# Optimization experiments

Hardware: AMD Instinct MI355X
Metric: run time of the kernel (lower is better)

## Reference

```python
import jax, jax.numpy as jnp
import numpy as np

B, T, D = 2, 4096, 768
H = 12
HD = D // H  # 64
SCALE = 1.0 / np.sqrt(HD)


def setup_inputs() -> dict:
    key = jax.random.key(0)
    k1, k2, k3 = jax.random.split(key, 3)
    x = jax.random.normal(k1, (B, T, D), dtype=jnp.float32)
    W_qkv = jax.random.normal(k2, (D, 3 * D), dtype=jnp.float32) * (1.0 / np.sqrt(D))
    b_qkv = jnp.zeros((3 * D,), dtype=jnp.float32)
    W_out = jax.random.normal(k3, (D, D), dtype=jnp.float32) * (1.0 / np.sqrt(D))
    b_out = jnp.zeros((D,), dtype=jnp.float32)
    return {"x": x, "W_qkv": W_qkv, "b_qkv": b_qkv, "W_out": W_out, "b_out": b_out}


def reference(x, W_qkv, b_qkv, W_out, b_out):
    Bx, Tx, C = x.shape
    qkv = x @ W_qkv + b_qkv                                  # [B,T,3D]
    qkv = qkv.reshape(Bx, Tx, 3, H, HD).transpose(2, 0, 3, 1, 4)  # [3,B,H,T,hd]
    q, k, v = qkv[0], qkv[1], qkv[2]
    scores = jnp.einsum('bhqd,bhkd->bhqk', q, k) * SCALE      # [B,H,T,T]
    causal = jnp.tril(jnp.ones((Tx, Tx), dtype=bool))
    scores = jnp.where(causal[None, None], scores, -jnp.inf)
    attn = jax.nn.softmax(scores, axis=-1)
    out = jnp.einsum('bhqk,bhkd->bhqd', attn, v)              # [B,H,T,hd]
    out = out.transpose(0, 2, 1, 3).reshape(Bx, Tx, C)        # [B,T,D]
    return out @ W_out + b_out
```

## Files before the change

kernel.cpp:

```cpp
#include <hip/hip_runtime.h>
#include <cstdint>
#include <cstddef>

typedef _Float16 f16x8 __attribute__((ext_vector_type(8)));
typedef _Float16 f16x4 __attribute__((ext_vector_type(4)));
typedef float    f32x4 __attribute__((ext_vector_type(4)));

#define AS_GLOBAL __attribute__((address_space(1)))
#define AS_LDS    __attribute__((address_space(3)))

__device__ __forceinline__ void load16_to_lds(const _Float16* g, _Float16* l) {
    __builtin_amdgcn_global_load_lds((const AS_GLOBAL void*)g, (AS_LDS void*)l, 16, 0, 0);
}

#define BB   2
#define TT   4096
#define DD   768
#define NH   12
#define HDIM 64
#define D3   2304
#define SC2  (0.125f * 1.44269504088896f)

__global__ __launch_bounds__(256) void prep(const float* __restrict__ x,
                                            _Float16* __restrict__ Xh,
                                            const float* __restrict__ Wqkv,
                                            _Float16* __restrict__ Wqkvt,
                                            const float* __restrict__ Wout,
                                            _Float16* __restrict__ Wot) {
    const int bid = blockIdx.x, tid = threadIdx.x;
    if (bid < 6144) {
        const int i = bid * 1024 + tid * 4;
        float4 v = *(const float4*)(x + i);
        f16x4 h;
        h[0] = (_Float16)v.x; h[1] = (_Float16)v.y;
        h[2] = (_Float16)v.z; h[3] = (_Float16)v.w;
        *(f16x4*)(Xh + i) = h;
        return;
    }
    __shared__ float tile[32][33];
    const float* in; _Float16* out; int C, bx, by;
    if (bid < 7872) {
        const int t = bid - 6144;
        in = Wqkv; out = Wqkvt; C = 2304;
        bx = (t % 72) * 32; by = (t / 72) * 32;
    } else {
        const int t = bid - 7872;
        in = Wout; out = Wot; C = 768;
        bx = (t % 24) * 32; by = (t / 24) * 32;
    }
    const int R = 768;
    const int tx = tid & 31, ty = tid >> 5;
#pragma unroll
    for (int j = 0; j < 32; j += 8)
        tile[ty + j][tx] = in[(size_t)(by + ty + j) * C + bx + tx];
    __syncthreads();
#pragma unroll
    for (int j = 0; j < 32; j += 8)
        out[(size_t)(bx + ty + j) * R + by + tx] = (_Float16)tile[tx][ty + j];
}

template <typename OutT>
__device__ __forceinline__ void gemm_body(const _Float16* __restrict__ A,
                                          const _Float16* __restrict__ Bt,
                                          const float* __restrict__ bias, bool bias_row,
                                          OutT* __restrict__ C, int N, int K,
                                          int m0, int n0,
                                          _Float16* As, _Float16* Bs) {
    const int tid  = threadIdx.x;
    const int wave = tid >> 6, lane = tid & 63, quad = lane >> 4, l16 = lane & 15;
    const int wm = (wave & 1) * 64, wn = (wave >> 1) * 64;
    const int rowc = lane >> 2, part = lane & 3;

    f32x4 acc[4][4];
#pragma unroll
    for (int i = 0; i < 4; ++i)
#pragma unroll
        for (int n = 0; n < 4; ++n) acc[i][n] = f32x4{0.f, 0.f, 0.f, 0.f};

    for (int k0 = 0; k0 < K; k0 += 32) {
        __syncthreads();
#pragma unroll
        for (int cc = 0; cc < 2; ++cc) {
            const int ch = wave * 2 + cc;
            load16_to_lds(A  + (size_t)(m0 + ch * 16 + rowc) * K + k0 + part * 8,
                          As + ch * 512);
            load16_to_lds(Bt + (size_t)(n0 + ch * 16 + rowc) * K + k0 + part * 8,
                          Bs + ch * 512);
        }
        __syncthreads();
#pragma unroll
        for (int i = 0; i < 4; ++i) {
            f16x8 a = *(const f16x8*)(As + (wm + i * 16 + l16) * 32 + quad * 8);
#pragma unroll
            for (int n = 0; n < 4; ++n) {
                f16x8 b = *(const f16x8*)(Bs + (wn + n * 16 + l16) * 32 + quad * 8);
                acc[i][n] = __builtin_amdgcn_mfma_f32_16x16x32_f16(a, b, acc[i][n], 0, 0, 0);
            }
        }
    }
#pragma unroll
    for (int i = 0; i < 4; ++i)
#pragma unroll
        for (int n = 0; n < 4; ++n)
#pragma unroll
            for (int r = 0; r < 4; ++r) {
                const int row = m0 + wm + i * 16 + quad * 4 + r;
                const int col = n0 + wn + n * 16 + l16;
                const float bv = bias_row ? bias[row] : bias[col];
                C[(size_t)row * N + col] = (OutT)(acc[i][n][r] + bv);
            }
}

__global__ __launch_bounds__(256) void gemm_qkv(const _Float16* __restrict__ Xh,
                                                const _Float16* __restrict__ Wqkvt,
                                                const float* __restrict__ bqkv,
                                                _Float16* __restrict__ QKh,
                                                _Float16* __restrict__ VtG) {
    __shared__ __align__(16) _Float16 As[128 * 32];
    __shared__ __align__(16) _Float16 Bs[128 * 32];
    const int bid = blockIdx.x;
    if (bid < 768) {
        const int bx = bid % 12, by = bid / 12;
        gemm_body<_Float16>(Xh, Wqkvt, bqkv, false, QKh, 1536, DD,
                            by * 128, bx * 128, As, Bs);
    } else {
        const int t = bid - 768;
        const int bx = t % 64, by = t / 64;
        gemm_body<_Float16>(Wqkvt + (size_t)1536 * DD, Xh, bqkv + 1536, true, VtG,
                            8192, DD, by * 128, bx * 128, As, Bs);
    }
}

__global__ __launch_bounds__(256) void gemm_out(const _Float16* __restrict__ A,
                                                const _Float16* __restrict__ Bt,
                                                const float* __restrict__ bias,
                                                float* __restrict__ C) {
    __shared__ __align__(16) _Float16 As[128 * 32];
    __shared__ __align__(16) _Float16 Bs[128 * 32];
    gemm_body<float>(A, Bt, bias, false, C, DD, DD,
                     (int)blockIdx.y * 128, (int)blockIdx.x * 128, As, Bs);
}

__global__ __launch_bounds__(128) void attn_kernel(const _Float16* __restrict__ qk,
                                                   const _Float16* __restrict__ vt,
                                                   _Float16* __restrict__ ao) {
    __shared__ __align__(16) _Float16 Ks[2][64 * 64];
    __shared__ __align__(16) _Float16 Vs[2][64 * 64];
    __shared__ __align__(16) _Float16 Ps[2][32 * 64];
    const int b = blockIdx.z, h = blockIdx.y;
    const int tid = threadIdx.x;
    const int wave = tid >> 6, lane = tid & 63, quad = lane >> 4, l16 = lane & 15;

    f16x8 ones;
#pragma unroll
    for (int j = 0; j < 8; ++j) ones[j] = (_Float16)1.0f;

    const _Float16* pK[4];
    const _Float16* pV[4];
#pragma unroll
    for (int p = 0; p < 4; ++p) {
        const int j  = wave * 32 + p * 8 + (lane >> 3);
        const int sig = (j & 15) * 4 + (j >> 4);
        const int cdk = (lane & 7) ^ (j & 7);
        pK[p] = qk + (size_t)(b * TT + sig) * 1536 + DD + h * HDIM + cdk * 8;
        pV[p] = vt + (size_t)(h * HDIM + j) * 8192 + b * TT + cdk * 8;
    }
    auto stage = [&](int buf, int k0) {
#pragma unroll
        for (int p = 0; p < 4; ++p) {
            load16_to_lds(pK[p] + (size_t)k0 * 1536, Ks[buf] + (wave * 32 + p * 8) * 64);
            load16_to_lds(pV[p] + k0,                Vs[buf] + (wave * 32 + p * 8) * 64);
        }
    };

    _Float16* pw[2][4];
#pragma unroll
    for (int mi = 0; mi < 2; ++mi)
#pragma unroll
        for (int r = 0; r < 4; ++r) {
            const int row = mi * 16 + quad * 4 + r;
            pw[mi][r] = Ps[wave] + row * 64 + (((l16 >> 1) ^ (row & 7)) * 8) + (l16 & 1) * 4;
        }
    const _Float16* pr[2][2];
#pragma unroll
    for (int mi = 0; mi < 2; ++mi)
#pragma unroll
        for (int kh = 0; kh < 2; ++kh) {
            const int row = mi * 16 + l16;
            pr[mi][kh] = Ps[wave] + row * 64 + (((kh * 4 + quad) ^ (row & 7)) * 8);
        }

    auto process = [&](int qt) {
        const int q0 = qt * 64;
        const int nkt = qt + 1;
        f16x8 aq[2][2];
#pragma unroll
        for (int mi = 0; mi < 2; ++mi) {
            const int q = q0 + wave * 32 + mi * 16 + l16;
            const _Float16* qp = qk + (size_t)(b * TT + q) * 1536 + h * HDIM + quad * 8;
            const _Float16 sc = (_Float16)SC2;
            aq[mi][0] = *(const f16x8*)qp * sc;
            aq[mi][1] = *(const f16x8*)(qp + 32) * sc;
        }
        f32x4 o[2][4], lac[2];
#pragma unroll
        for (int mi = 0; mi < 2; ++mi) {
#pragma unroll
            for (int n = 0; n < 4; ++n) o[mi][n] = f32x4{0.f, 0.f, 0.f, 0.f};
            lac[mi] = f32x4{0.f, 0.f, 0.f, 0.f};
        }

        __syncthreads();
        stage(0, 0);
        int cur = 0;
        for (int kt = 0; kt < nkt; ++kt) {
            __syncthreads();
            if (kt + 1 < nkt) stage(cur ^ 1, (kt + 1) * 64);

            f32x4 s[2][4];
#pragma unroll
            for (int mi = 0; mi < 2; ++mi)
#pragma unroll
                for (int n = 0; n < 4; ++n) s[mi][n] = f32x4{0.f, 0.f, 0.f, 0.f};
#pragma unroll
            for (int kh = 0; kh < 2; ++kh)
#pragma unroll
                for (int n = 0; n < 4; ++n) {
                    const int pos = (kh * 4 + quad) ^ (l16 & 7);
                    f16x8 bk = *(const f16x8*)(Ks[cur] + (n * 16 + l16) * 64 + pos * 8);
#pragma unroll
                    for (int mi = 0; mi < 2; ++mi)
                        s[mi][n] = __builtin_amdgcn_mfma_f32_16x16x32_f16(aq[mi][kh], bk,
                                                                          s[mi][n], 0, 0, 0);
                }

            if (kt == nkt - 1) {
#pragma unroll
                for (int n = 0; n < 4; ++n) {
                    const int kg = kt * 64 + l16 * 4 + n;
#pragma unroll
                    for (int mi = 0; mi < 2; ++mi) {
                        const int qg = q0 + wave * 32 + mi * 16 + quad * 4;
#pragma unroll
                        for (int r = 0; r < 4; ++r)
                            if (kg > qg + r) s[mi][n][r] = -1e30f;
                    }
                }
            }

#pragma unroll
            for (int mi = 0; mi < 2; ++mi)
#pragma unroll
                for (int r = 0; r < 4; ++r) {
                    f16x4 pk;
#pragma unroll
                    for (int n = 0; n < 4; ++n)
                        pk[n] = (_Float16)__builtin_amdgcn_exp2f(s[mi][n][r]);
                    *(f16x4*)pw[mi][r] = pk;
                }

#pragma unroll
            for (int kh = 0; kh < 2; ++kh) {
                f16x8 ap[2];
#pragma unroll
                for (int mi = 0; mi < 2; ++mi) {
                    ap[mi] = *(const f16x8*)pr[mi][kh];
                    lac[mi] = __builtin_amdgcn_mfma_f32_16x16x32_f16(ap[mi], ones,
                                                                     lac[mi], 0, 0, 0);
                }
#pragma unroll
                for (int n = 0; n < 4; ++n) {
                    const int posv = (kh * 4 + quad) ^ (l16 & 7);
                    f16x8 bv = *(const f16x8*)(Vs[cur] + (n * 16 + l16) * 64 + posv * 8);
#pragma unroll
                    for (int mi = 0; mi < 2; ++mi)
                        o[mi][n] = __builtin_amdgcn_mfma_f32_16x16x32_f16(ap[mi], bv,
                                                                          o[mi][n], 0, 0, 0);
                }
            }
            cur ^= 1;
        }

#pragma unroll
        for (int mi = 0; mi < 2; ++mi)
#pragma unroll
            for (int r = 0; r < 4; ++r) {
                const float inv = 1.0f / lac[mi][r];
                const int q = q0 + wave * 32 + mi * 16 + quad * 4 + r;
#pragma unroll
                for (int n = 0; n < 4; ++n) {
                    const int col = h * HDIM + n * 16 + l16;
                    ao[(size_t)(b * TT + q) * DD + col] = (_Float16)(o[mi][n][r] * inv);
                }
            }
    };

    process(63 - blockIdx.x);
    process(blockIdx.x);
}

extern "C" void kernel_launch(void* const* d_in, const int* in_sizes, int n_in,
                              void* d_out, int out_size, void* d_ws, size_t ws_size,
                              hipStream_t stream) {
    const float* x     = (const float*)d_in[0];
    const float* Wqkv  = (const float*)d_in[1];
    const float* bqkv  = (const float*)d_in[2];
    const float* Wout  = (const float*)d_in[3];
    const float* bout  = (const float*)d_in[4];
    float* out = (float*)d_out;

    char* ws = (char*)d_ws;
    _Float16* Xh    = (_Float16*)ws;  ws += (size_t)BB * TT * DD * 2;
    _Float16* Wqkvt = (_Float16*)ws;  ws += (size_t)D3 * DD * 2;
    _Float16* Wot   = (_Float16*)ws;  ws += (size_t)DD * DD * 2;
    _Float16* QKh   = (_Float16*)ws;  ws += (size_t)BB * TT * 1536 * 2;
    _Float16* VtG   = (_Float16*)ws;  ws += (size_t)DD * BB * TT * 2;
    _Float16* AOh   = (_Float16*)ws;  ws += (size_t)BB * TT * DD * 2;

    prep<<<8448, 256, 0, stream>>>(x, Xh, Wqkv, Wqkvt, Wout, Wot);

    gemm_qkv<<<1152, 256, 0, stream>>>(Xh, Wqkvt, bqkv, QKh, VtG);

    attn_kernel<<<dim3(32, NH, BB), 128, 0, stream>>>(QKh, VtG, AOh);

    gemm_out<<<dim3(DD / 128, (BB * TT) / 128), 256, 0, stream>>>(AOh, Wot, bout, out);
}
```

Measured before the change: 259.9 us.

## Widen GEMM K-step to 64 and make attention single-wave with direct K/V loads

```diff
diff --git a/kernel.cpp b/kernel.cpp
--- a/kernel.cpp
+++ b/kernel.cpp
@@ -69,7 +69,7 @@
     const int tid  = threadIdx.x;
     const int wave = tid >> 6, lane = tid & 63, quad = lane >> 4, l16 = lane & 15;
     const int wm = (wave & 1) * 64, wn = (wave >> 1) * 64;
-    const int rowc = lane >> 2, part = lane & 3;
+    const int rowc = lane >> 3, part = lane & 7;
 
     f32x4 acc[4][4];
 #pragma unroll
@@ -77,24 +77,27 @@
 #pragma unroll
         for (int n = 0; n < 4; ++n) acc[i][n] = f32x4{0.f, 0.f, 0.f, 0.f};
 
-    for (int k0 = 0; k0 < K; k0 += 32) {
+    for (int k0 = 0; k0 < K; k0 += 64) {
         __syncthreads();
 #pragma unroll
-        for (int cc = 0; cc < 2; ++cc) {
-            const int ch = wave * 2 + cc;
-            load16_to_lds(A  + (size_t)(m0 + ch * 16 + rowc) * K + k0 + part * 8,
+        for (int cc = 0; cc < 4; ++cc) {
+            const int ch = wave * 4 + cc;
+            load16_to_lds(A  + (size_t)(m0 + ch * 8 + rowc) * K + k0 + part * 8,
                           As + ch * 512);
-            load16_to_lds(Bt + (size_t)(n0 + ch * 16 + rowc) * K + k0 + part * 8,
+            load16_to_lds(Bt + (size_t)(n0 + ch * 8 + rowc) * K + k0 + part * 8,
                           Bs + ch * 512);
         }
         __syncthreads();
 #pragma unroll
         for (int i = 0; i < 4; ++i) {
-            f16x8 a = *(const f16x8*)(As + (wm + i * 16 + l16) * 32 + quad * 8);
+            f16x8 a0 = *(const f16x8*)(As + (wm + i * 16 + l16) * 64 + quad * 8);
+            f16x8 a1 = *(const f16x8*)(As + (wm + i * 16 + l16) * 64 + 32 + quad * 8);
 #pragma unroll
             for (int n = 0; n < 4; ++n) {
-                f16x8 b = *(const f16x8*)(Bs + (wn + n * 16 + l16) * 32 + quad * 8);
-                acc[i][n] = __builtin_amdgcn_mfma_f32_16x16x32_f16(a, b, acc[i][n], 0, 0, 0);
+                f16x8 b0 = *(const f16x8*)(Bs + (wn + n * 16 + l16) * 64 + quad * 8);
+                f16x8 b1 = *(const f16x8*)(Bs + (wn + n * 16 + l16) * 64 + 32 + quad * 8);
+                acc[i][n] = __builtin_amdgcn_mfma_f32_16x16x32_f16(a0, b0, acc[i][n], 0, 0, 0);
+                acc[i][n] = __builtin_amdgcn_mfma_f32_16x16x32_f16(a1, b1, acc[i][n], 0, 0, 0);
             }
         }
     }
@@ -116,8 +119,8 @@
                                                 const float* __restrict__ bqkv,
                                                 _Float16* __restrict__ QKh,
                                                 _Float16* __restrict__ VtG) {
-    __shared__ __align__(16) _Float16 As[128 * 32];
-    __shared__ __align__(16) _Float16 Bs[128 * 32];
+    __shared__ __align__(16) _Float16 As[128 * 64];
+    __shared__ __align__(16) _Float16 Bs[128 * 64];
     const int bid = blockIdx.x;
     if (bid < 768) {
         const int bx = bid % 12, by = bid / 12;
@@ -135,43 +138,26 @@
                                                 const _Float16* __restrict__ Bt,
                                                 const float* __restrict__ bias,
                                                 float* __restrict__ C) {
-    __shared__ __align__(16) _Float16 As[128 * 32];
-    __shared__ __align__(16) _Float16 Bs[128 * 32];
+    __shared__ __align__(16) _Float16 As[128 * 64];
+    __shared__ __align__(16) _Float16 Bs[128 * 64];
     gemm_body<float>(A, Bt, bias, false, C, DD, DD,
                      (int)blockIdx.y * 128, (int)blockIdx.x * 128, As, Bs);
 }
 
-__global__ __launch_bounds__(128) void attn_kernel(const _Float16* __restrict__ qk,
-                                                   const _Float16* __restrict__ vt,
-                                                   _Float16* __restrict__ ao) {
-    __shared__ __align__(16) _Float16 Ks[2][64 * 64];
-    __shared__ __align__(16) _Float16 Vs[2][64 * 64];
-    __shared__ __align__(16) _Float16 Ps[2][32 * 64];
+__global__ __launch_bounds__(64, 2) void attn_kernel(const _Float16* __restrict__ qk,
+                                                     const _Float16* __restrict__ vt,
+                                                     _Float16* __restrict__ ao) {
+    __shared__ __align__(16) _Float16 Ps[32 * 64];
     const int b = blockIdx.z, h = blockIdx.y;
-    const int tid = threadIdx.x;
-    const int wave = tid >> 6, lane = tid & 63, quad = lane >> 4, l16 = lane & 15;
+    const int lane = threadIdx.x;
+    const int quad = lane >> 4, l16 = lane & 15;
 
     f16x8 ones;
 #pragma unroll
     for (int j = 0; j < 8; ++j) ones[j] = (_Float16)1.0f;
 
-    const _Float16* pK[4];
-    const _Float16* pV[4];
-#pragma unroll
-    for (int p = 0; p < 4; ++p) {
-        const int j  = wave * 32 + p * 8 + (lane >> 3);
-        const int sig = (j & 15) * 4 + (j >> 4);
-        const int cdk = (lane & 7) ^ (j & 7);
-        pK[p] = qk + (size_t)(b * TT + sig) * 1536 + DD + h * HDIM + cdk * 8;
-        pV[p] = vt + (size_t)(h * HDIM + j) * 8192 + b * TT + cdk * 8;
-    }
-    auto stage = [&](int buf, int k0) {
-#pragma unroll
-        for (int p = 0; p < 4; ++p) {
-            load16_to_lds(pK[p] + (size_t)k0 * 1536, Ks[buf] + (wave * 32 + p * 8) * 64);
-            load16_to_lds(pV[p] + k0,                Vs[buf] + (wave * 32 + p * 8) * 64);
-        }
-    };
+    const _Float16* kbase = qk + ((size_t)(b * TT) + l16 * 4) * 1536 + DD + h * HDIM + quad * 8;
+    const _Float16* vbase = vt + ((size_t)(h * HDIM) + l16) * 8192 + b * TT + quad * 8;
 
     _Float16* pw[2][4];
 #pragma unroll
@@ -179,7 +165,7 @@
 #pragma unroll
         for (int r = 0; r < 4; ++r) {
             const int row = mi * 16 + quad * 4 + r;
-            pw[mi][r] = Ps[wave] + row * 64 + (((l16 >> 1) ^ (row & 7)) * 8) + (l16 & 1) * 4;
+            pw[mi][r] = Ps + row * 64 + (((l16 >> 1) ^ (row & 7)) * 8) + (l16 & 1) * 4;
         }
     const _Float16* pr[2][2];
 #pragma unroll
@@ -187,16 +173,16 @@
 #pragma unroll
         for (int kh = 0; kh < 2; ++kh) {
             const int row = mi * 16 + l16;
-            pr[mi][kh] = Ps[wave] + row * 64 + (((kh * 4 + quad) ^ (row & 7)) * 8);
-        }
-
-    auto process = [&](int qt) {
-        const int q0 = qt * 64;
-        const int nkt = qt + 1;
+            pr[mi][kh] = Ps + row * 64 + (((kh * 4 + quad) ^ (row & 7)) * 8);
+        }
+
+    auto process = [&](int tile) {
+        const int q0 = tile * 32;
+        const int nkt = (tile >> 1) + 1;
         f16x8 aq[2][2];
 #pragma unroll
         for (int mi = 0; mi < 2; ++mi) {
-            const int q = q0 + wave * 32 + mi * 16 + l16;
+            const int q = q0 + mi * 16 + l16;
             const _Float16* qp = qk + (size_t)(b * TT + q) * 1536 + h * HDIM + quad * 8;
             const _Float16 sc = (_Float16)SC2;
             aq[mi][0] = *(const f16x8*)qp * sc;
@@ -210,12 +196,18 @@
             lac[mi] = f32x4{0.f, 0.f, 0.f, 0.f};
         }
 
-        __syncthreads();
-        stage(0, 0);
-        int cur = 0;
         for (int kt = 0; kt < nkt; ++kt) {
-            __syncthreads();
-            if (kt + 1 < nkt) stage(cur ^ 1, (kt + 1) * 64);
+            const int k0 = kt * 64;
+            f16x8 bk[2][4], bv[2][4];
+            const _Float16* kb = kbase + (size_t)k0 * 1536;
+            const _Float16* vb = vbase + k0;
+#pragma unroll
+            for (int kh = 0; kh < 2; ++kh)
+#pragma unroll
+                for (int n = 0; n < 4; ++n) {
+                    bk[kh][n] = *(const f16x8*)(kb + (size_t)n * 1536 + kh * 32);
+                    bv[kh][n] = *(const f16x8*)(vb + (size_t)n * 16 * 8192 + kh * 32);
+                }
 
             f32x4 s[2][4];
 #pragma unroll
@@ -225,22 +217,19 @@
 #pragma unroll
             for (int kh = 0; kh < 2; ++kh)
 #pragma unroll
+                for (int n = 0; n < 4; ++n)
+#pragma unroll
+                    for (int mi = 0; mi < 2; ++mi)
+                        s[mi][n] = __builtin_amdgcn_mfma_f32_16x16x32_f16(aq[mi][kh], bk[kh][n],
+                                                                          s[mi][n], 0, 0, 0);
+
+            if (kt == nkt - 1) {
+#pragma unroll
                 for (int n = 0; n < 4; ++n) {
-                    const int pos = (kh * 4 + quad) ^ (l16 & 7);
-                    f16x8 bk = *(const f16x8*)(Ks[cur] + (n * 16 + l16) * 64 + pos * 8);
-#pragma unroll
-                    for (int mi = 0; mi < 2; ++mi)
-                        s[mi][n] = __builtin_amdgcn_mfma_f32_16x16x32_f16(aq[mi][kh], bk,
-                                                                          s[mi][n], 0, 0, 0);
-                }
-
-            if (kt == nkt - 1) {
-#pragma unroll
-                for (int n = 0; n < 4; ++n) {
-                    const int kg = kt * 64 + l16 * 4 + n;
+                    const int kg = k0 + l16 * 4 + n;
 #pragma unroll
                     for (int mi = 0; mi < 2; ++mi) {
-                        const int qg = q0 + wave * 32 + mi * 16 + quad * 4;
+                        const int qg = q0 + mi * 16 + quad * 4;
 #pragma unroll
                         for (int r = 0; r < 4; ++r)
                             if (kg > qg + r) s[mi][n][r] = -1e30f;
@@ -269,16 +258,12 @@
                                                                      lac[mi], 0, 0, 0);
                 }
 #pragma unroll
-                for (int n = 0; n < 4; ++n) {
-                    const int posv = (kh * 4 + quad) ^ (l16 & 7);
-                    f16x8 bv = *(const f16x8*)(Vs[cur] + (n * 16 + l16) * 64 + posv * 8);
+                for (int n = 0; n < 4; ++n)
 #pragma unroll
                     for (int mi = 0; mi < 2; ++mi)
-                        o[mi][n] = __builtin_amdgcn_mfma_f32_16x16x32_f16(ap[mi], bv,
+                        o[mi][n] = __builtin_amdgcn_mfma_f32_16x16x32_f16(ap[mi], bv[kh][n],
                                                                           o[mi][n], 0, 0, 0);
-                }
-            }
-            cur ^= 1;
+            }
         }
 
 #pragma unroll
@@ -286,7 +271,7 @@
 #pragma unroll
             for (int r = 0; r < 4; ++r) {
                 const float inv = 1.0f / lac[mi][r];
-                const int q = q0 + wave * 32 + mi * 16 + quad * 4 + r;
+                const int q = q0 + mi * 16 + quad * 4 + r;
 #pragma unroll
                 for (int n = 0; n < 4; ++n) {
                     const int col = h * HDIM + n * 16 + l16;
@@ -295,7 +280,7 @@
             }
     };
 
-    process(63 - blockIdx.x);
+    process(127 - blockIdx.x);
     process(blockIdx.x);
 }
 
@@ -321,7 +306,7 @@
 
     gemm_qkv<<<1152, 256, 0, stream>>>(Xh, Wqkvt, bqkv, QKh, VtG);
 
-    attn_kernel<<<dim3(32, NH, BB), 128, 0, stream>>>(QKh, VtG, AOh);
+    attn_kernel<<<dim3(64, NH, BB), 64, 0, stream>>>(QKh, VtG, AOh);
 
     gemm_out<<<dim3(DD / 128, (BB * TT) / 128), 256, 0, stream>>>(AOh, Wot, bout, out);
 }
```

New measurement: 404.4 us. 55.6% more time.
